# Kernel optimization log

Measured on AMD Instinct MI355X. Metric: run time of the kernel, lower is better.

The kernel has to match this reference:

```python
import jax, jax.numpy as jnp
import numpy as np

N, C, CI, H, W = 64, 512, 256, 12, 4
EPS = 1e-5


def _conv1x1(v, w, b=None):
    # v: [n, cin, h, w], w: [cout, cin]
    o = jnp.einsum('nchw,oc->nohw', v, w)
    if b is not None:
        o = o + b[None, :, None, None]
    return o


def _layernorm(v, g, b):
    # normalize over (C, H, W) per sample, affine params shaped [C, H, W]
    mu = v.mean(axis=(1, 2, 3), keepdims=True)
    var = v.var(axis=(1, 2, 3), keepdims=True)
    return (v - mu) / jnp.sqrt(var + EPS) * g[None] + b[None]


def setup_inputs() -> dict:
    key = jax.random.key(0)
    ks = jax.random.split(key, 12)
    s = 0.02
    return {
        'x': jax.random.normal(ks[0], (N, C, H, W), dtype=jnp.float32),
        'theta_w': jax.random.normal(ks[1], (CI, C), dtype=jnp.float32) * s,
        'theta_b': jnp.zeros((CI,), dtype=jnp.float32),
        'phi_w': jax.random.normal(ks[2], (CI, C), dtype=jnp.float32) * s,
        'phi_b': jnp.zeros((CI,), dtype=jnp.float32),
        'conv1_w': jax.random.normal(ks[3], (C, C), dtype=jnp.float32) * s,
        'conv2_w': jax.random.normal(ks[4], (C, C), dtype=jnp.float32) * s,
        'ln1_g': jnp.ones((C, H, W), dtype=jnp.float32),
        'ln1_b': jnp.zeros((C, H, W), dtype=jnp.float32),
        'ln2_g': jnp.ones((C, H, W), dtype=jnp.float32),
        'ln2_b': jnp.zeros((C, H, W), dtype=jnp.float32),
    }


def reference(x, theta_w, theta_b, phi_w, phi_b, conv1_w, conv2_w,
              ln1_g, ln1_b, ln2_g, ln2_b):
    n = x.shape[0]
    hw = H * W
    # 1x1 conv projections (conv is per-sample, so compute once on the N nodes
    # instead of on the N^2 gathered copies -- identical math)
    theta = _conv1x1(x, theta_w, theta_b)          # [N, CI, H, W]  (gallery proj)
    phi = _conv1x1(x, phi_w, phi_b)                # [N, CI, H, W]  (query proj)
    # MaxPool2d(2,2) on phi -> [N, CI, 6, 2] -> [N, CI, 12]
    phi_p = phi.reshape(n, CI, H // 2, 2, W // 2, 2).max(axis=(3, 5))
    phi_p = phi_p.reshape(n, CI, -1)               # [N, CI, 12]
    t = theta.reshape(n, CI, hw).transpose(0, 2, 1)  # [N, HW, CI]
    # f[i, j] = theta(x[j]) @ pooled phi(x[i]), norm='size' divides by 12
    f = jnp.einsum('jsc,icm->ijsm', t, phi_p) / phi_p.shape[-1]  # [Nq, Ng, HW, 12]
    m = f.max(axis=-1)                             # [Nq, Ng, HW]; max instead of softmax-sum
    # all-pairs layout p = i*N + j: qs[p] = i, gs[p] = j (torch.where row-major)
    gs = jnp.tile(jnp.arange(n), n)                # [N*N]
    # masked gallery image z = x[gs] * attention map, then scatter_add over gs
    z = x[gs] * m.reshape(n * n, 1, H, W)          # [N*N, C, H, W]
    x2 = jax.ops.segment_sum(z, gs, num_segments=n)
    # postprocessing (dropouts are identity at p=0)
    x = x2 + x                                     # res1
    x = _layernorm(x, ln1_g, ln1_b)
    h = _conv1x1(jax.nn.relu(_conv1x1(x, conv1_w)), conv2_w)
    x = x + h                                      # res2
    x = _layernorm(x, ln2_g, ln2_b)
    return x
```

## Files before the change

kernel.cpp:

```cpp
#include <hip/hip_runtime.h>
#include <hip/hip_bf16.h>

#define NN 64
#define CC 512
#define HW 48
#define LNSZ (CC * HW)

typedef __attribute__((ext_vector_type(8))) short bf16x8;
typedef __attribute__((ext_vector_type(4))) float floatx4;

static const size_t WB_OFF   = 0;
static const size_t BC_OFF   = 393216;
static const size_t S_OFF    = 393728;
static const size_t CXP_OFF  = 396928;
static const size_t CX2_OFF  = 409216;
static const size_t ST2_OFF  = 421504;
static const size_t XB_OFF   = 422016;
static const size_t TP_OFF   = 1208448;
static const size_t YB_OFF   = 1994880;
static const size_t UB_OFF   = 2781312;
static const size_t PP_OFF   = 3567744;
static const size_t YY_OFF   = 3666048;
static const size_t VV_OFF   = 5238912;

__device__ __forceinline__ void block_reduce2(float& sum, float& sq) {
  const int lane = threadIdx.x & 63, w = threadIdx.x >> 6;
#pragma unroll
  for (int off = 32; off > 0; off >>= 1) {
    sum += __shfl_down(sum, off, 64);
    sq  += __shfl_down(sq, off, 64);
  }
  __shared__ float rs[4], rq[4];
  if (lane == 0) { rs[w] = sum; rq[w] = sq; }
  __syncthreads();
  if (threadIdx.x == 0) {
    sum = rs[0] + rs[1] + rs[2] + rs[3];
    sq  = rq[0] + rq[1] + rq[2] + rq[3];
  }
}

__global__ __launch_bounds__(256) void prep_all(
    const float* __restrict__ tw, const float* __restrict__ pw,
    const float* __restrict__ c1, const float* __restrict__ c2,
    const float* __restrict__ tb, const float* __restrict__ pb,
    const float* __restrict__ x,
    __hip_bfloat16* __restrict__ Wb, float* __restrict__ bcat,
    float* __restrict__ S, __hip_bfloat16* __restrict__ xb,
    float* __restrict__ cxp, float* __restrict__ cx2p) {
  __shared__ float ts[128 * 49];
  __shared__ float ps[192], pq[192];
  if (blockIdx.x < 768) {
    int g = blockIdx.x * 256 + threadIdx.x;
    float4 v;
    if (g < 32768)       v = ((const float4*)tw)[g];
    else if (g < 65536)  v = ((const float4*)pw)[g - 32768];
    else if (g < 131072) v = ((const float4*)c1)[g - 65536];
    else                 v = ((const float4*)c2)[g - 131072];
    union { short4 s4; __hip_bfloat16 h[4]; } u;
    u.h[0] = __float2bfloat16(v.x);
    u.h[1] = __float2bfloat16(v.y);
    u.h[2] = __float2bfloat16(v.z);
    u.h[3] = __float2bfloat16(v.w);
    ((short4*)Wb)[g] = u.s4;
    if (g < 64)       ((float4*)bcat)[g] = ((const float4*)tb)[g];
    else if (g < 128) ((float4*)bcat)[g] = ((const float4*)pb)[g - 64];
    if (g < 768) ((float4*)S)[g] = make_float4(0.f, 0.f, 0.f, 0.f);
    return;
  }
  const int bb = blockIdx.x - 768;
  const int bx = bb & 3;
  const int n  = bb >> 2;
  const int t  = threadIdx.x;
  const float* src = x + (size_t)n * LNSZ + (size_t)bx * 128 * HW;
#pragma unroll
  for (int k = 0; k < 6; ++k) {
    int idx = t + k * 256;
    float4 v = ((const float4*)src)[idx];
    int c = idx / 12, sq = (idx % 12) * 4;
    float* d = ts + c * 49 + sq;
    d[0] = v.x; d[1] = v.y; d[2] = v.z; d[3] = v.w;
  }
  __syncthreads();
  if (t < 192) {
    int s = t % 48, q = t / 48;
    float sum = 0.f, sq2 = 0.f;
#pragma unroll
    for (int c = q * 32; c < q * 32 + 32; ++c) {
      float v = ts[c * 49 + s];
      sum += v; sq2 += v * v;
    }
    ps[t] = sum; pq[t] = sq2;
  }
  __hip_bfloat16* dst = xb + (size_t)n * LNSZ + bx * 128;
#pragma unroll
  for (int k = 0; k < 12; ++k) {
    int idx = t + k * 256;
    int s = idx >> 6, cp = idx & 63;
    __hip_bfloat162 p;
    p.x = __float2bfloat16(ts[(cp * 2) * 49 + s]);
    p.y = __float2bfloat16(ts[(cp * 2 + 1) * 49 + s]);
    *(__hip_bfloat162*)(dst + (size_t)s * 512 + cp * 2) = p;
  }
  __syncthreads();
  if (t < 48) {
    cxp[((size_t)n * 4 + bx) * 48 + t] = ps[t] + ps[48 + t] + ps[96 + t] + ps[144 + t];
    cx2p[((size_t)n * 4 + bx) * 48 + t] = pq[t] + pq[48 + t] + pq[96 + t] + pq[144 + t];
  }
}

__global__ __launch_bounds__(256) void gemm_bf16out(
    const __hip_bfloat16* __restrict__ Wb, const __hip_bfloat16* __restrict__ inb,
    const float* __restrict__ bias, __hip_bfloat16* __restrict__ outb, int relu,
    __hip_bfloat16* __restrict__ Pp) {
  const int oc = blockIdx.x, n = blockIdx.y;
  const int w = threadIdx.x >> 6, lane = threadIdx.x & 63;
  const int c16 = lane & 15, quad = lane >> 4;
  const int obase = oc * 128 + w * 32;

  const __hip_bfloat16* A0 = Wb + (size_t)(obase + c16) * 512 + quad * 8;
  const __hip_bfloat16* A1 = A0 + 16 * 512;
  const __hip_bfloat16* B0 = inb + (size_t)n * LNSZ + (size_t)c16 * 512 + quad * 8;

  floatx4 zero = {0.f, 0.f, 0.f, 0.f};
  floatx4 acc[2][3];
#pragma unroll
  for (int i = 0; i < 2; ++i)
#pragma unroll
    for (int j = 0; j < 3; ++j) acc[i][j] = zero;

  bf16x8 a[2], b[3];
  a[0] = *(const bf16x8*)(A0);
  a[1] = *(const bf16x8*)(A1);
  b[0] = *(const bf16x8*)(B0);
  b[1] = *(const bf16x8*)(B0 + 16 * 512);
  b[2] = *(const bf16x8*)(B0 + 32 * 512);

  for (int k = 0; k < 480; k += 32) {
    bf16x8 an[2], bn[3];
    const int k2 = k + 32;
    an[0] = *(const bf16x8*)(A0 + k2);
    an[1] = *(const bf16x8*)(A1 + k2);
    bn[0] = *(const bf16x8*)(B0 + k2);
    bn[1] = *(const bf16x8*)(B0 + 16 * 512 + k2);
    bn[2] = *(const bf16x8*)(B0 + 32 * 512 + k2);
#pragma unroll
    for (int i = 0; i < 2; ++i)
#pragma unroll
      for (int j = 0; j < 3; ++j)
        acc[i][j] = __builtin_amdgcn_mfma_f32_16x16x32_bf16(a[i], b[j],
                                                            acc[i][j], 0, 0, 0);
    a[0] = an[0]; a[1] = an[1];
    b[0] = bn[0]; b[1] = bn[1]; b[2] = bn[2];
  }
#pragma unroll
  for (int i = 0; i < 2; ++i)
#pragma unroll
    for (int j = 0; j < 3; ++j)
      acc[i][j] = __builtin_amdgcn_mfma_f32_16x16x32_bf16(a[i], b[j],
                                                          acc[i][j], 0, 0, 0);

  __shared__ float pt[128 * 49];
  const int do_pp = (Pp != nullptr) && (oc >= 2);

  __hip_bfloat16* on = outb + (size_t)n * LNSZ;
#pragma unroll
  for (int i = 0; i < 2; ++i) {
    const int o0 = obase + i * 16 + quad * 4;
    float bv[4];
#pragma unroll
    for (int r = 0; r < 4; ++r) bv[r] = bias ? bias[o0 + r] : 0.f;
#pragma unroll
    for (int j = 0; j < 3; ++j) {
      const int s = j * 16 + c16;
      union { short4 s4; __hip_bfloat16 h[4]; } u;
#pragma unroll
      for (int r = 0; r < 4; ++r) {
        float v = acc[i][j][r] + bv[r];
        if (relu) v = fmaxf(v, 0.f);
        u.h[r] = __float2bfloat16(v);
        if (do_pp) pt[(w * 32 + i * 16 + quad * 4 + r) * 49 + s] = v;
      }
      *(short4*)(on + (size_t)s * 512 + o0) = u.s4;
    }
  }
  if (do_pp) {
    __syncthreads();
#pragma unroll
    for (int rep = 0; rep < 6; ++rep) {
      int idx = threadIdx.x + rep * 256;
      int m = idx >> 7, cil = idx & 127;
      int sb = (m >> 1) * 8 + (m & 1) * 2;
      const float* pr = pt + cil * 49;
      float mx = fmaxf(fmaxf(pr[sb], pr[sb + 1]), fmaxf(pr[sb + 4], pr[sb + 5]));
      Pp[((size_t)(n * 12 + m) << 8) + (oc - 2) * 128 + cil] = __float2bfloat16(mx);
    }
  }
}

__global__ __launch_bounds__(256) void dgemm_fused(
    const __hip_bfloat16* __restrict__ A, const __hip_bfloat16* __restrict__ B,
    float* __restrict__ S) {
  const int bn = blockIdx.x * 48;
  const int w = threadIdx.x >> 6, lane = threadIdx.x & 63;
  const int c16 = lane & 15, quad = lane >> 4;
  const int bm = blockIdx.y * 128 + w * 32;

  const __hip_bfloat16* A0 = A + (size_t)(bm + c16) * 512 + quad * 8;
  const __hip_bfloat16* A1 = A0 + 16 * 512;
  const __hip_bfloat16* Bp = B + (size_t)(bn + c16) * 256 + quad * 8;

  floatx4 zero = {0.f, 0.f, 0.f, 0.f};
  floatx4 acc[2][3];
#pragma unroll
  for (int i = 0; i < 2; ++i)
#pragma unroll
    for (int j = 0; j < 3; ++j) acc[i][j] = zero;

#pragma unroll 2
  for (int k = 0; k < 256; k += 32) {
    bf16x8 a0 = *(const bf16x8*)(A0 + k);
    bf16x8 a1 = *(const bf16x8*)(A1 + k);
    bf16x8 b0 = *(const bf16x8*)(Bp + k);
    bf16x8 b1 = *(const bf16x8*)(Bp + 16 * 256 + k);
    bf16x8 b2 = *(const bf16x8*)(Bp + 32 * 256 + k);
    acc[0][0] = __builtin_amdgcn_mfma_f32_16x16x32_bf16(a0, b0, acc[0][0], 0, 0, 0);
    acc[0][1] = __builtin_amdgcn_mfma_f32_16x16x32_bf16(a0, b1, acc[0][1], 0, 0, 0);
    acc[0][2] = __builtin_amdgcn_mfma_f32_16x16x32_bf16(a0, b2, acc[0][2], 0, 0, 0);
    acc[1][0] = __builtin_amdgcn_mfma_f32_16x16x32_bf16(a1, b0, acc[1][0], 0, 0, 0);
    acc[1][1] = __builtin_amdgcn_mfma_f32_16x16x32_bf16(a1, b1, acc[1][1], 0, 0, 0);
    acc[1][2] = __builtin_amdgcn_mfma_f32_16x16x32_bf16(a1, b2, acc[1][2], 0, 0, 0);
  }

  __shared__ float red[4 * 48 * 33];
  float* rw = red + w * (48 * 33);
#pragma unroll
  for (int i = 0; i < 2; ++i)
#pragma unroll
    for (int j = 0; j < 3; ++j)
#pragma unroll
      for (int r = 0; r < 4; ++r)
        rw[(j * 16 + c16) * 33 + (i * 16 + quad * 4 + r)] = acc[i][j][r];
  __syncthreads();
  if (lane < 32) {
    float sum = 0.f;
#pragma unroll
    for (int grp = 0; grp < 4; ++grp) {
      float mx = rw[(grp * 12) * 33 + lane];
#pragma unroll
      for (int m = 1; m < 12; ++m)
        mx = fmaxf(mx, rw[(grp * 12 + m) * 33 + lane]);
      sum += mx;
    }
    atomicAdd(&S[bm + lane], sum * (1.0f / 12.0f));
  }
}

__global__ __launch_bounds__(256) void ln1_norm_tr(
    const float* __restrict__ x, const float* __restrict__ S,
    const float* __restrict__ cxp, const float* __restrict__ cx2p,
    const float* __restrict__ g, const float* __restrict__ b,
    float* __restrict__ y, __hip_bfloat16* __restrict__ yb) {
  const int bx = blockIdx.x, n = blockIdx.y, t = threadIdx.x;
  __shared__ float ts[128 * 49];
  __shared__ float sS[HW];
  __shared__ float sstat[2];
  if (t < HW) sS[t] = 1.0f + S[n * HW + t];
  if (t < 64) {
    float sum = 0.f, sq = 0.f;
    if (t < 48) {
      float a = 1.0f + S[n * HW + t];
      float c1 = 0.f, c2 = 0.f;
#pragma unroll
      for (int ch = 0; ch < 4; ++ch) {
        c1 += cxp[((size_t)n * 4 + ch) * 48 + t];
        c2 += cx2p[((size_t)n * 4 + ch) * 48 + t];
      }
      sum = a * c1;
      sq = a * a * c2;
    }
#pragma unroll
    for (int off = 32; off > 0; off >>= 1) {
      sum += __shfl_down(sum, off, 64);
      sq  += __shfl_down(sq, off, 64);
    }
    if (t == 0) {
      float mu = sum * (1.0f / LNSZ);
      float var = sq * (1.0f / LNSZ) - mu * mu;
      sstat[0] = mu;
      sstat[1] = 1.0f / sqrtf(var + 1e-5f);
    }
  }
  __syncthreads();
  const float mu = sstat[0], rstd = sstat[1];
  const size_t chunk = (size_t)bx * 6144;
  const float* xn = x + (size_t)n * LNSZ + chunk;
  float* yn = y + (size_t)n * LNSZ + chunk;
  const float* gp = g + chunk;
  const float* bp = b + chunk;
#pragma unroll
  for (int k = 0; k < 6; ++k) {
    int idx = t + k * 256;
    int c = idx / 12, sq0 = (idx % 12) * 4;
    float4 xv = ((const float4*)xn)[idx];
    float4 gv = ((const float4*)gp)[idx];
    float4 bv = ((const float4*)bp)[idx];
    float4 o;
    o.x = (xv.x * sS[sq0]     - mu) * rstd * gv.x + bv.x;
    o.y = (xv.y * sS[sq0 + 1] - mu) * rstd * gv.y + bv.y;
    o.z = (xv.z * sS[sq0 + 2] - mu) * rstd * gv.z + bv.z;
    o.w = (xv.w * sS[sq0 + 3] - mu) * rstd * gv.w + bv.w;
    ((float4*)yn)[idx] = o;
    float* d = ts + c * 49 + sq0;
    d[0] = o.x; d[1] = o.y; d[2] = o.z; d[3] = o.w;
  }
  __syncthreads();
  __hip_bfloat16* dst = yb + (size_t)n * LNSZ + bx * 128;
#pragma unroll
  for (int k = 0; k < 12; ++k) {
    int idx = t + k * 256;
    int s = idx >> 6, cp = idx & 63;
    __hip_bfloat162 p;
    p.x = __float2bfloat16(ts[(cp * 2) * 49 + s]);
    p.y = __float2bfloat16(ts[(cp * 2 + 1) * 49 + s]);
    *(__hip_bfloat162*)(dst + (size_t)s * 512 + cp * 2) = p;
  }
}

__global__ __launch_bounds__(256) void conv2_fused(
    const __hip_bfloat16* __restrict__ Wb, const __hip_bfloat16* __restrict__ inb,
    const float* __restrict__ y, float* __restrict__ v,
    float2* __restrict__ stats2) {
  const int oc = blockIdx.x, n = blockIdx.y;
  const int w = threadIdx.x >> 6, lane = threadIdx.x & 63;
  const int c16 = lane & 15, quad = lane >> 4;
  const int obase = oc * 128 + w * 32;

  const __hip_bfloat16* A0 = Wb + (size_t)(obase + c16) * 512 + quad * 8;
  const __hip_bfloat16* A1 = A0 + 16 * 512;
  const __hip_bfloat16* B0 = inb + (size_t)n * LNSZ + (size_t)c16 * 512 + quad * 8;

  floatx4 zero = {0.f, 0.f, 0.f, 0.f};
  floatx4 acc[2][3];
#pragma unroll
  for (int i = 0; i < 2; ++i)
#pragma unroll
    for (int j = 0; j < 3; ++j) acc[i][j] = zero;

  bf16x8 a[2], b[3];
  a[0] = *(const bf16x8*)(A0);
  a[1] = *(const bf16x8*)(A1);
  b[0] = *(const bf16x8*)(B0);
  b[1] = *(const bf16x8*)(B0 + 16 * 512);
  b[2] = *(const bf16x8*)(B0 + 32 * 512);

  for (int k = 0; k < 480; k += 32) {
    bf16x8 an[2], bn[3];
    const int k2 = k + 32;
    an[0] = *(const bf16x8*)(A0 + k2);
    an[1] = *(const bf16x8*)(A1 + k2);
    bn[0] = *(const bf16x8*)(B0 + k2);
    bn[1] = *(const bf16x8*)(B0 + 16 * 512 + k2);
    bn[2] = *(const bf16x8*)(B0 + 32 * 512 + k2);
#pragma unroll
    for (int i = 0; i < 2; ++i)
#pragma unroll
      for (int j = 0; j < 3; ++j)
        acc[i][j] = __builtin_amdgcn_mfma_f32_16x16x32_bf16(a[i], b[j],
                                                            acc[i][j], 0, 0, 0);
    a[0] = an[0]; a[1] = an[1];
    b[0] = bn[0]; b[1] = bn[1]; b[2] = bn[2];
  }
#pragma unroll
  for (int i = 0; i < 2; ++i)
#pragma unroll
    for (int j = 0; j < 3; ++j)
      acc[i][j] = __builtin_amdgcn_mfma_f32_16x16x32_bf16(a[i], b[j],
                                                          acc[i][j], 0, 0, 0);

  const float* yn = y + (size_t)n * LNSZ;
  float* vn = v + (size_t)n * LNSZ;
  float sum = 0.f, sq = 0.f;
#pragma unroll
  for (int i = 0; i < 2; ++i)
#pragma unroll
    for (int r = 0; r < 4; ++r) {
      const int o = obase + i * 16 + quad * 4 + r;
#pragma unroll
      for (int j = 0; j < 3; ++j) {
        const int s = j * 16 + c16;
        float val = acc[i][j][r] + yn[(size_t)o * HW + s];
        vn[(size_t)o * HW + s] = val;
        sum += val;
        sq += val * val;
      }
    }
  block_reduce2(sum, sq);
  if (threadIdx.x == 0) stats2[n * 4 + oc] = make_float2(sum, sq);
}

__global__ __launch_bounds__(256) void ln2_norm(
    const float* __restrict__ v, const float2* __restrict__ stats2,
    const float* __restrict__ g2, const float* __restrict__ b2,
    float* __restrict__ out) {
  const int bx = blockIdx.x, n = blockIdx.y, t = threadIdx.x;
  __shared__ float smu, srstd;
  if (t == 0) {
    float s1 = 0.f, s2 = 0.f;
#pragma unroll
    for (int k = 0; k < 4; ++k) {
      float2 p = stats2[n * 4 + k];
      s1 += p.x; s2 += p.y;
    }
    float mu = s1 * (1.0f / LNSZ);
    float var = s2 * (1.0f / LNSZ) - mu * mu;
    smu = mu;
    srstd = 1.0f / sqrtf(var + 1e-5f);
  }
  __syncthreads();
  const float mu = smu, rstd = srstd;
  const size_t chunk = (size_t)bx * 6144;
  const float* vn = v + (size_t)n * LNSZ + chunk;
  float* on = out + (size_t)n * LNSZ + chunk;
  const float* gp = g2 + chunk;
  const float* bp = b2 + chunk;
#pragma unroll
  for (int k = 0; k < 6; ++k) {
    int idx = t + k * 256;
    float4 vv = ((const float4*)vn)[idx];
    float4 gv = ((const float4*)gp)[idx];
    float4 bv = ((const float4*)bp)[idx];
    float4 o;
    o.x = (vv.x - mu) * rstd * gv.x + bv.x;
    o.y = (vv.y - mu) * rstd * gv.y + bv.y;
    o.z = (vv.z - mu) * rstd * gv.z + bv.z;
    o.w = (vv.w - mu) * rstd * gv.w + bv.w;
    ((float4*)on)[idx] = o;
  }
}

extern "C" void kernel_launch(void* const* d_in, const int* in_sizes, int n_in,
                              void* d_out, int out_size, void* d_ws, size_t ws_size,
                              hipStream_t stream) {
  const float* x   = (const float*)d_in[0];
  const float* tw  = (const float*)d_in[1];
  const float* tb  = (const float*)d_in[2];
  const float* pw  = (const float*)d_in[3];
  const float* pb  = (const float*)d_in[4];
  const float* c1w = (const float*)d_in[5];
  const float* c2w = (const float*)d_in[6];
  const float* g1  = (const float*)d_in[7];
  const float* b1  = (const float*)d_in[8];
  const float* g2  = (const float*)d_in[9];
  const float* b2  = (const float*)d_in[10];

  float* ws = (float*)d_ws;
  __hip_bfloat16* Wb = (__hip_bfloat16*)(ws + WB_OFF);
  float* bcat        = ws + BC_OFF;
  float* S           = ws + S_OFF;
  float* cxp         = ws + CXP_OFF;
  float* cx2p        = ws + CX2_OFF;
  float2* st2        = (float2*)(ws + ST2_OFF);
  __hip_bfloat16* xb = (__hip_bfloat16*)(ws + XB_OFF);
  __hip_bfloat16* tp = (__hip_bfloat16*)(ws + TP_OFF);
  __hip_bfloat16* yb = (__hip_bfloat16*)(ws + YB_OFF);
  __hip_bfloat16* ub = (__hip_bfloat16*)(ws + UB_OFF);
  __hip_bfloat16* Pp = (__hip_bfloat16*)(ws + PP_OFF);
  float* y           = ws + YY_OFF;
  float* v           = ws + VV_OFF;
  float* out         = (float*)d_out;

  prep_all<<<1024, 256, 0, stream>>>(tw, pw, c1w, c2w, tb, pb, x,
                                     Wb, bcat, S, xb, cxp, cx2p);
  gemm_bf16out<<<dim3(4, NN), 256, 0, stream>>>(Wb, xb, bcat, tp, 0, Pp);
  dgemm_fused<<<dim3(16, 24), 256, 0, stream>>>(tp, Pp, S);
  ln1_norm_tr<<<dim3(4, NN), 256, 0, stream>>>(x, S, cxp, cx2p, g1, b1, y, yb);
  gemm_bf16out<<<dim3(4, NN), 256, 0, stream>>>(Wb + 512 * 512, yb, nullptr, ub, 1,
                                                nullptr);
  conv2_fused<<<dim3(4, NN), 256, 0, stream>>>(Wb + 1024 * 512, ub, y, v, st2);
  ln2_norm<<<dim3(4, NN), 256, 0, stream>>>(v, st2, g2, b2, out);
}
```

Before: 135.9 us.

## Split K across two wave groups in GEMM kernels with LDS reduction

Doubles block size to 512 threads in the three projection/conv GEMMs and the pairwise dgemm, splitting the K dimension between two groups of four waves and summing the partial accumulators through shared memory. The aim is to shorten each wave's serial MFMA/load chain and raise occupancy, since the grids of 256 and 384 blocks underfill the GPU. In exchange it adds an LDS round trip and extra barriers, and the block reduction is widened to eight waves.

```diff
diff --git a/kernel.cpp b/kernel.cpp
--- a/kernel.cpp
+++ b/kernel.cpp
@@ -23,19 +23,19 @@
 static const size_t YY_OFF   = 3666048;
 static const size_t VV_OFF   = 5238912;
 
-__device__ __forceinline__ void block_reduce2(float& sum, float& sq) {
+__device__ __forceinline__ void block_reduce2_8(float& sum, float& sq) {
   const int lane = threadIdx.x & 63, w = threadIdx.x >> 6;
 #pragma unroll
   for (int off = 32; off > 0; off >>= 1) {
     sum += __shfl_down(sum, off, 64);
     sq  += __shfl_down(sq, off, 64);
   }
-  __shared__ float rs[4], rq[4];
+  __shared__ float rs[8], rq[8];
   if (lane == 0) { rs[w] = sum; rq[w] = sq; }
   __syncthreads();
   if (threadIdx.x == 0) {
-    sum = rs[0] + rs[1] + rs[2] + rs[3];
-    sq  = rq[0] + rq[1] + rq[2] + rq[3];
+    sum = rs[0] + rs[1] + rs[2] + rs[3] + rs[4] + rs[5] + rs[6] + rs[7];
+    sq  = rq[0] + rq[1] + rq[2] + rq[3] + rq[4] + rq[5] + rq[6] + rq[7];
   }
 }
 
@@ -108,18 +108,19 @@
   }
 }
 
-__global__ __launch_bounds__(256) void gemm_bf16out(
+__global__ __launch_bounds__(512) void gemm_bf16out(
     const __hip_bfloat16* __restrict__ Wb, const __hip_bfloat16* __restrict__ inb,
     const float* __restrict__ bias, __hip_bfloat16* __restrict__ outb, int relu,
     __hip_bfloat16* __restrict__ Pp) {
   const int oc = blockIdx.x, n = blockIdx.y;
   const int w = threadIdx.x >> 6, lane = threadIdx.x & 63;
+  const int wo = w & 3, wk = w >> 2;
   const int c16 = lane & 15, quad = lane >> 4;
-  const int obase = oc * 128 + w * 32;
-
-  const __hip_bfloat16* A0 = Wb + (size_t)(obase + c16) * 512 + quad * 8;
+  const int obase = oc * 128 + wo * 32;
+
+  const __hip_bfloat16* A0 = Wb + (size_t)(obase + c16) * 512 + wk * 256 + quad * 8;
   const __hip_bfloat16* A1 = A0 + 16 * 512;
-  const __hip_bfloat16* B0 = inb + (size_t)n * LNSZ + (size_t)c16 * 512 + quad * 8;
+  const __hip_bfloat16* B0 = inb + (size_t)n * LNSZ + (size_t)c16 * 512 + wk * 256 + quad * 8;
 
   floatx4 zero = {0.f, 0.f, 0.f, 0.f};
   floatx4 acc[2][3];
@@ -135,7 +136,7 @@
   b[1] = *(const bf16x8*)(B0 + 16 * 512);
   b[2] = *(const bf16x8*)(B0 + 32 * 512);
 
-  for (int k = 0; k < 480; k += 32) {
+  for (int k = 0; k < 224; k += 32) {
     bf16x8 an[2], bn[3];
     const int k2 = k + 32;
     an[0] = *(const bf16x8*)(A0 + k2);
@@ -159,55 +160,80 @@
       acc[i][j] = __builtin_amdgcn_mfma_f32_16x16x32_bf16(a[i], b[j],
                                                           acc[i][j], 0, 0, 0);
 
-  __shared__ float pt[128 * 49];
+  __shared__ float buf[6400];
+  if (wk == 1) {
+    float* dst = buf + wo * 1600;
+#pragma unroll
+    for (int i = 0; i < 2; ++i)
+#pragma unroll
+      for (int j = 0; j < 3; ++j)
+#pragma unroll
+        for (int r = 0; r < 4; ++r)
+          dst[(i * 16 + quad * 4 + r) * 49 + (j * 16 + c16)] = acc[i][j][r];
+  }
+  __syncthreads();
   const int do_pp = (Pp != nullptr) && (oc >= 2);
-
-  __hip_bfloat16* on = outb + (size_t)n * LNSZ;
-#pragma unroll
-  for (int i = 0; i < 2; ++i) {
-    const int o0 = obase + i * 16 + quad * 4;
-    float bv[4];
-#pragma unroll
-    for (int r = 0; r < 4; ++r) bv[r] = bias ? bias[o0 + r] : 0.f;
-#pragma unroll
-    for (int j = 0; j < 3; ++j) {
-      const int s = j * 16 + c16;
-      union { short4 s4; __hip_bfloat16 h[4]; } u;
-#pragma unroll
-      for (int r = 0; r < 4; ++r) {
-        float v = acc[i][j][r] + bv[r];
-        if (relu) v = fmaxf(v, 0.f);
-        u.h[r] = __float2bfloat16(v);
-        if (do_pp) pt[(w * 32 + i * 16 + quad * 4 + r) * 49 + s] = v;
+  if (wk == 0) {
+    const float* src = buf + wo * 1600;
+#pragma unroll
+    for (int i = 0; i < 2; ++i)
+#pragma unroll
+      for (int j = 0; j < 3; ++j)
+#pragma unroll
+        for (int r = 0; r < 4; ++r)
+          acc[i][j][r] += src[(i * 16 + quad * 4 + r) * 49 + (j * 16 + c16)];
+  }
+  if (do_pp) __syncthreads();
+
+  if (wk == 0) {
+    __hip_bfloat16* on = outb + (size_t)n * LNSZ;
+#pragma unroll
+    for (int i = 0; i < 2; ++i) {
+      const int o0 = obase + i * 16 + quad * 4;
+      float bv[4];
+#pragma unroll
+      for (int r = 0; r < 4; ++r) bv[r] = bias ? bias[o0 + r] : 0.f;
+#pragma unroll
+      for (int j = 0; j < 3; ++j) {
+        const int s = j * 16 + c16;
+        union { short4 s4; __hip_bfloat16 h[4]; } u;
+#pragma unroll
+        for (int r = 0; r < 4; ++r) {
+          float v = acc[i][j][r] + bv[r];
+          if (relu) v = fmaxf(v, 0.f);
+          u.h[r] = __float2bfloat16(v);
+          if (do_pp) buf[(wo * 32 + i * 16 + quad * 4 + r) * 49 + s] = v;
+        }
+        *(short4*)(on + (size_t)s * 512 + o0) = u.s4;
       }
-      *(short4*)(on + (size_t)s * 512 + o0) = u.s4;
     }
   }
   if (do_pp) {
     __syncthreads();
 #pragma unroll
-    for (int rep = 0; rep < 6; ++rep) {
-      int idx = threadIdx.x + rep * 256;
+    for (int rep = 0; rep < 3; ++rep) {
+      int idx = threadIdx.x + rep * 512;
       int m = idx >> 7, cil = idx & 127;
       int sb = (m >> 1) * 8 + (m & 1) * 2;
-      const float* pr = pt + cil * 49;
+      const float* pr = buf + cil * 49;
       float mx = fmaxf(fmaxf(pr[sb], pr[sb + 1]), fmaxf(pr[sb + 4], pr[sb + 5]));
       Pp[((size_t)(n * 12 + m) << 8) + (oc - 2) * 128 + cil] = __float2bfloat16(mx);
     }
   }
 }
 
-__global__ __launch_bounds__(256) void dgemm_fused(
+__global__ __launch_bounds__(512) void dgemm_fused(
     const __hip_bfloat16* __restrict__ A, const __hip_bfloat16* __restrict__ B,
     float* __restrict__ S) {
   const int bn = blockIdx.x * 48;
   const int w = threadIdx.x >> 6, lane = threadIdx.x & 63;
+  const int wo = w & 3, wk = w >> 2;
   const int c16 = lane & 15, quad = lane >> 4;
-  const int bm = blockIdx.y * 128 + w * 32;
-
-  const __hip_bfloat16* A0 = A + (size_t)(bm + c16) * 512 + quad * 8;
+  const int bm = blockIdx.y * 128 + wo * 32;
+
+  const __hip_bfloat16* A0 = A + (size_t)(bm + c16) * 512 + wk * 128 + quad * 8;
   const __hip_bfloat16* A1 = A0 + 16 * 512;
-  const __hip_bfloat16* Bp = B + (size_t)(bn + c16) * 256 + quad * 8;
+  const __hip_bfloat16* Bp = B + (size_t)(bn + c16) * 256 + wk * 128 + quad * 8;
 
   floatx4 zero = {0.f, 0.f, 0.f, 0.f};
   floatx4 acc[2][3];
@@ -216,8 +242,8 @@
 #pragma unroll
     for (int j = 0; j < 3; ++j) acc[i][j] = zero;
 
-#pragma unroll 2
-  for (int k = 0; k < 256; k += 32) {
+#pragma unroll
+  for (int k = 0; k < 128; k += 32) {
     bf16x8 a0 = *(const bf16x8*)(A0 + k);
     bf16x8 a1 = *(const bf16x8*)(A1 + k);
     bf16x8 b0 = *(const bf16x8*)(Bp + k);
@@ -232,16 +258,28 @@
   }
 
   __shared__ float red[4 * 48 * 33];
-  float* rw = red + w * (48 * 33);
-#pragma unroll
-  for (int i = 0; i < 2; ++i)
-#pragma unroll
-    for (int j = 0; j < 3; ++j)
-#pragma unroll
-      for (int r = 0; r < 4; ++r)
-        rw[(j * 16 + c16) * 33 + (i * 16 + quad * 4 + r)] = acc[i][j][r];
-  __syncthreads();
-  if (lane < 32) {
+  float* rw = red + wo * (48 * 33);
+  if (wk == 1) {
+#pragma unroll
+    for (int i = 0; i < 2; ++i)
+#pragma unroll
+      for (int j = 0; j < 3; ++j)
+#pragma unroll
+        for (int r = 0; r < 4; ++r)
+          rw[(j * 16 + c16) * 33 + (i * 16 + quad * 4 + r)] = acc[i][j][r];
+  }
+  __syncthreads();
+  if (wk == 0) {
+#pragma unroll
+    for (int i = 0; i < 2; ++i)
+#pragma unroll
+      for (int j = 0; j < 3; ++j)
+#pragma unroll
+        for (int r = 0; r < 4; ++r)
+          rw[(j * 16 + c16) * 33 + (i * 16 + quad * 4 + r)] += acc[i][j][r];
+  }
+  __syncthreads();
+  if (wk == 0 && lane < 32) {
     float sum = 0.f;
 #pragma unroll
     for (int grp = 0; grp < 4; ++grp) {
@@ -326,18 +364,19 @@
   }
 }
 
-__global__ __launch_bounds__(256) void conv2_fused(
+__global__ __launch_bounds__(512) void conv2_fused(
     const __hip_bfloat16* __restrict__ Wb, const __hip_bfloat16* __restrict__ inb,
     const float* __restrict__ y, float* __restrict__ v,
     float2* __restrict__ stats2) {
   const int oc = blockIdx.x, n = blockIdx.y;
   const int w = threadIdx.x >> 6, lane = threadIdx.x & 63;
+  const int wo = w & 3, wk = w >> 2;
   const int c16 = lane & 15, quad = lane >> 4;
-  const int obase = oc * 128 + w * 32;
-
-  const __hip_bfloat16* A0 = Wb + (size_t)(obase + c16) * 512 + quad * 8;
+  const int obase = oc * 128 + wo * 32;
+
+  const __hip_bfloat16* A0 = Wb + (size_t)(obase + c16) * 512 + wk * 256 + quad * 8;
   const __hip_bfloat16* A1 = A0 + 16 * 512;
-  const __hip_bfloat16* B0 = inb + (size_t)n * LNSZ + (size_t)c16 * 512 + quad * 8;
+  const __hip_bfloat16* B0 = inb + (size_t)n * LNSZ + (size_t)c16 * 512 + wk * 256 + quad * 8;
 
   floatx4 zero = {0.f, 0.f, 0.f, 0.f};
   floatx4 acc[2][3];
@@ -353,7 +392,7 @@
   b[1] = *(const bf16x8*)(B0 + 16 * 512);
   b[2] = *(const bf16x8*)(B0 + 32 * 512);
 
-  for (int k = 0; k < 480; k += 32) {
+  for (int k = 0; k < 224; k += 32) {
     bf16x8 an[2], bn[3];
     const int k2 = k + 32;
     an[0] = *(const bf16x8*)(A0 + k2);
@@ -377,24 +416,46 @@
       acc[i][j] = __builtin_amdgcn_mfma_f32_16x16x32_bf16(a[i], b[j],
                                                           acc[i][j], 0, 0, 0);
 
-  const float* yn = y + (size_t)n * LNSZ;
-  float* vn = v + (size_t)n * LNSZ;
+  __shared__ float buf[6400];
+  if (wk == 1) {
+    float* dst = buf + wo * 1600;
+#pragma unroll
+    for (int i = 0; i < 2; ++i)
+#pragma unroll
+      for (int j = 0; j < 3; ++j)
+#pragma unroll
+        for (int r = 0; r < 4; ++r)
+          dst[(i * 16 + quad * 4 + r) * 49 + (j * 16 + c16)] = acc[i][j][r];
+  }
+  __syncthreads();
   float sum = 0.f, sq = 0.f;
-#pragma unroll
-  for (int i = 0; i < 2; ++i)
-#pragma unroll
-    for (int r = 0; r < 4; ++r) {
-      const int o = obase + i * 16 + quad * 4 + r;
-#pragma unroll
-      for (int j = 0; j < 3; ++j) {
-        const int s = j * 16 + c16;
-        float val = acc[i][j][r] + yn[(size_t)o * HW + s];
-        vn[(size_t)o * HW + s] = val;
-        sum += val;
-        sq += val * val;
+  if (wk == 0) {
+    const float* src = buf + wo * 1600;
+#pragma unroll
+    for (int i = 0; i < 2; ++i)
+#pragma unroll
+      for (int j = 0; j < 3; ++j)
+#pragma unroll
+        for (int r = 0; r < 4; ++r)
+          acc[i][j][r] += src[(i * 16 + quad * 4 + r) * 49 + (j * 16 + c16)];
+    const float* yn = y + (size_t)n * LNSZ;
+    float* vn = v + (size_t)n * LNSZ;
+#pragma unroll
+    for (int i = 0; i < 2; ++i)
+#pragma unroll
+      for (int r = 0; r < 4; ++r) {
+        const int o = obase + i * 16 + quad * 4 + r;
+#pragma unroll
+        for (int j = 0; j < 3; ++j) {
+          const int s = j * 16 + c16;
+          float val = acc[i][j][r] + yn[(size_t)o * HW + s];
+          vn[(size_t)o * HW + s] = val;
+          sum += val;
+          sq += val * val;
+        }
       }
-    }
-  block_reduce2(sum, sq);
+  }
+  block_reduce2_8(sum, sq);
   if (threadIdx.x == 0) stats2[n * 4 + oc] = make_float2(sum, sq);
 }
 
@@ -471,11 +532,11 @@
 
   prep_all<<<1024, 256, 0, stream>>>(tw, pw, c1w, c2w, tb, pb, x,
                                      Wb, bcat, S, xb, cxp, cx2p);
-  gemm_bf16out<<<dim3(4, NN), 256, 0, stream>>>(Wb, xb, bcat, tp, 0, Pp);
-  dgemm_fused<<<dim3(16, 24), 256, 0, stream>>>(tp, Pp, S);
+  gemm_bf16out<<<dim3(4, NN), 512, 0, stream>>>(Wb, xb, bcat, tp, 0, Pp);
+  dgemm_fused<<<dim3(16, 24), 512, 0, stream>>>(tp, Pp, S);
   ln1_norm_tr<<<dim3(4, NN), 256, 0, stream>>>(x, S, cxp, cx2p, g1, b1, y, yb);
-  gemm_bf16out<<<dim3(4, NN), 256, 0, stream>>>(Wb + 512 * 512, yb, nullptr, ub, 1,
+  gemm_bf16out<<<dim3(4, NN), 512, 0, stream>>>(Wb + 512 * 512, yb, nullptr, ub, 1,
                                                 nullptr);
-  conv2_fused<<<dim3(4, NN), 256, 0, stream>>>(Wb + 1024 * 512, ub, y, v, st2);
+  conv2_fused<<<dim3(4, NN), 512, 0, stream>>>(Wb + 1024 * 512, ub, y, v, st2);
   ln2_norm<<<dim3(4, NN), 256, 0, stream>>>(v, st2, g2, b2, out);
 }
```

Measured after the change: 139.6 us. 1.03x slower.

## Fuse LN2 normalization into conv2 epilogue via per-sample atomic barrier

Applied to the files above, without the earlier changes.

Merges the final layernorm into the conv2 GEMM kernel. The four blocks of each sample publish partial sums, bump an atomic counter and spin until all four have arrived, then normalize their register-resident outputs directly. This removes one kernel launch and the write and re-read of the intermediate v buffer. In exchange it relies on all 256 blocks being co-resident to avoid deadlock, and it adds spin-wait latency. The counter is zeroed in prep_all by extending the existing zeroing range.

```diff
diff --git a/kernel.cpp b/kernel.cpp
--- a/kernel.cpp
+++ b/kernel.cpp
@@ -12,6 +12,7 @@
 static const size_t WB_OFF   = 0;
 static const size_t BC_OFF   = 393216;
 static const size_t S_OFF    = 393728;
+static const size_t CNT_OFF  = 396800;
 static const size_t CXP_OFF  = 396928;
 static const size_t CX2_OFF  = 409216;
 static const size_t ST2_OFF  = 421504;
@@ -21,7 +22,6 @@
 static const size_t UB_OFF   = 2781312;
 static const size_t PP_OFF   = 3567744;
 static const size_t YY_OFF   = 3666048;
-static const size_t VV_OFF   = 5238912;
 
 __device__ __forceinline__ void block_reduce2(float& sum, float& sq) {
   const int lane = threadIdx.x & 63, w = threadIdx.x >> 6;
@@ -64,7 +64,7 @@
     ((short4*)Wb)[g] = u.s4;
     if (g < 64)       ((float4*)bcat)[g] = ((const float4*)tb)[g];
     else if (g < 128) ((float4*)bcat)[g] = ((const float4*)pb)[g - 64];
-    if (g < 768) ((float4*)S)[g] = make_float4(0.f, 0.f, 0.f, 0.f);
+    if (g < 784) ((float4*)S)[g] = make_float4(0.f, 0.f, 0.f, 0.f);
     return;
   }
   const int bb = blockIdx.x - 768;
@@ -326,10 +326,11 @@
   }
 }
 
-__global__ __launch_bounds__(256) void conv2_fused(
+__global__ __launch_bounds__(256) void conv2_ln2(
     const __hip_bfloat16* __restrict__ Wb, const __hip_bfloat16* __restrict__ inb,
-    const float* __restrict__ y, float* __restrict__ v,
-    float2* __restrict__ stats2) {
+    const float* __restrict__ y, const float* __restrict__ g2,
+    const float* __restrict__ b2, float2* __restrict__ stats2,
+    int* __restrict__ cnt, float* __restrict__ out) {
   const int oc = blockIdx.x, n = blockIdx.y;
   const int w = threadIdx.x >> 6, lane = threadIdx.x & 63;
   const int c16 = lane & 15, quad = lane >> 4;
@@ -378,7 +379,6 @@
                                                           acc[i][j], 0, 0, 0);
 
   const float* yn = y + (size_t)n * LNSZ;
-  float* vn = v + (size_t)n * LNSZ;
   float sum = 0.f, sq = 0.f;
 #pragma unroll
   for (int i = 0; i < 2; ++i)
@@ -389,53 +389,53 @@
       for (int j = 0; j < 3; ++j) {
         const int s = j * 16 + c16;
         float val = acc[i][j][r] + yn[(size_t)o * HW + s];
-        vn[(size_t)o * HW + s] = val;
+        acc[i][j][r] = val;
         sum += val;
         sq += val * val;
       }
     }
   block_reduce2(sum, sq);
-  if (threadIdx.x == 0) stats2[n * 4 + oc] = make_float2(sum, sq);
-}
-
-__global__ __launch_bounds__(256) void ln2_norm(
-    const float* __restrict__ v, const float2* __restrict__ stats2,
-    const float* __restrict__ g2, const float* __restrict__ b2,
-    float* __restrict__ out) {
-  const int bx = blockIdx.x, n = blockIdx.y, t = threadIdx.x;
-  __shared__ float smu, srstd;
-  if (t == 0) {
+
+  __shared__ float sstat[2];
+  if (threadIdx.x == 0) {
+    stats2[n * 4 + oc] = make_float2(sum, sq);
+    __threadfence();
+    atomicAdd(&cnt[n], 1);
+    while (__hip_atomic_load(&cnt[n], __ATOMIC_ACQUIRE,
+                             __HIP_MEMORY_SCOPE_AGENT) < 4)
+      __builtin_amdgcn_s_sleep(2);
     float s1 = 0.f, s2 = 0.f;
 #pragma unroll
     for (int k = 0; k < 4; ++k) {
-      float2 p = stats2[n * 4 + k];
+      unsigned long long pk = __hip_atomic_load(
+          (const unsigned long long*)&stats2[n * 4 + k], __ATOMIC_RELAXED,
+          __HIP_MEMORY_SCOPE_AGENT);
+      float2 p = *(float2*)&pk;
       s1 += p.x; s2 += p.y;
     }
     float mu = s1 * (1.0f / LNSZ);
     float var = s2 * (1.0f / LNSZ) - mu * mu;
-    smu = mu;
-    srstd = 1.0f / sqrtf(var + 1e-5f);
-  }
-  __syncthreads();
-  const float mu = smu, rstd = srstd;
-  const size_t chunk = (size_t)bx * 6144;
-  const float* vn = v + (size_t)n * LNSZ + chunk;
-  float* on = out + (size_t)n * LNSZ + chunk;
-  const float* gp = g2 + chunk;
-  const float* bp = b2 + chunk;
-#pragma unroll
-  for (int k = 0; k < 6; ++k) {
-    int idx = t + k * 256;
-    float4 vv = ((const float4*)vn)[idx];
-    float4 gv = ((const float4*)gp)[idx];
-    float4 bv = ((const float4*)bp)[idx];
-    float4 o;
-    o.x = (vv.x - mu) * rstd * gv.x + bv.x;
-    o.y = (vv.y - mu) * rstd * gv.y + bv.y;
-    o.z = (vv.z - mu) * rstd * gv.z + bv.z;
-    o.w = (vv.w - mu) * rstd * gv.w + bv.w;
-    ((float4*)on)[idx] = o;
-  }
+    sstat[0] = mu;
+    sstat[1] = 1.0f / sqrtf(var + 1e-5f);
+  }
+  __syncthreads();
+  const float mu = sstat[0], rstd = sstat[1];
+
+  float* on = out + (size_t)n * LNSZ;
+  const float* g2n = g2;
+  const float* b2n = b2;
+#pragma unroll
+  for (int i = 0; i < 2; ++i)
+#pragma unroll
+    for (int r = 0; r < 4; ++r) {
+      const int o = obase + i * 16 + quad * 4 + r;
+#pragma unroll
+      for (int j = 0; j < 3; ++j) {
+        const int s = j * 16 + c16;
+        const size_t idx = (size_t)o * HW + s;
+        on[idx] = (acc[i][j][r] - mu) * rstd * g2n[idx] + b2n[idx];
+      }
+    }
 }
 
 extern "C" void kernel_launch(void* const* d_in, const int* in_sizes, int n_in,
@@ -457,6 +457,7 @@
   __hip_bfloat16* Wb = (__hip_bfloat16*)(ws + WB_OFF);
   float* bcat        = ws + BC_OFF;
   float* S           = ws + S_OFF;
+  int* cnt           = (int*)(ws + CNT_OFF);
   float* cxp         = ws + CXP_OFF;
   float* cx2p        = ws + CX2_OFF;
   float2* st2        = (float2*)(ws + ST2_OFF);
@@ -466,7 +467,6 @@
   __hip_bfloat16* ub = (__hip_bfloat16*)(ws + UB_OFF);
   __hip_bfloat16* Pp = (__hip_bfloat16*)(ws + PP_OFF);
   float* y           = ws + YY_OFF;
-  float* v           = ws + VV_OFF;
   float* out         = (float*)d_out;
 
   prep_all<<<1024, 256, 0, stream>>>(tw, pw, c1w, c2w, tb, pb, x,
@@ -476,6 +476,6 @@
   ln1_norm_tr<<<dim3(4, NN), 256, 0, stream>>>(x, S, cxp, cx2p, g1, b1, y, yb);
   gemm_bf16out<<<dim3(4, NN), 256, 0, stream>>>(Wb + 512 * 512, yb, nullptr, ub, 1,
                                                 nullptr);
-  conv2_fused<<<dim3(4, NN), 256, 0, stream>>>(Wb + 1024 * 512, ub, y, v, st2);
-  ln2_norm<<<dim3(4, NN), 256, 0, stream>>>(v, st2, g2, b2, out);
-}
+  conv2_ln2<<<dim3(4, NN), 256, 0, stream>>>(Wb + 1024 * 512, ub, y, g2, b2,
+                                             st2, cnt, out);
+}
```

New measurement: 140.5 us. 3.4% more time.
